# Performance work log

Measured on AMD Instinct MI355X. Metric: run time of the kernel, lower is better.

## Reference

```python
import jax, jax.numpy as jnp
import numpy as np

N = 100000   # num_nodes
E = 1600000  # num_edges
D = 64       # input_dim
H = 64       # hidden_dim
G = 64       # num graphs in batch


def gcn_conv(x, row, col, ew, W, b):
    """PyG GCNConv with edge_weight and self-loops (weight 1.0).
    out = D^{-1/2} (A + I) D^{-1/2} X W + b, aggregating src->dst (row->col)."""
    h = x @ W  # [N, H]
    deg = jax.ops.segment_sum(ew, col, num_segments=N) + 1.0  # self-loop weight 1
    dinv = jnp.where(deg > 0, jax.lax.rsqrt(deg), 0.0)
    norm = dinv[row] * ew * dinv[col]                     # [E]
    agg = jax.ops.segment_sum(h[row] * norm[:, None], col, num_segments=N)
    out = agg + h * (dinv * dinv)[:, None]                # self-loop term
    return out + b


def setup_inputs() -> dict:
    key = jax.random.key(0)
    ks = jax.random.split(key, 20)
    def w(i, shape, fan_in):
        return (jax.random.uniform(ks[i], shape, jnp.float32) * 2.0 - 1.0) / np.sqrt(fan_in)
    inp = {
        "x": jax.random.normal(ks[0], (N, D), jnp.float32),
        "edge_index": jax.random.randint(ks[1], (2, E), 0, N, dtype=jnp.int64),
        "edge_attr": jax.random.uniform(ks[2], (E, 1), jnp.float32),
        "batch": jnp.sort(jax.random.randint(ks[3], (N,), 0, G, dtype=jnp.int64)),
        # GCN layers
        "W0": w(4, (D, H), D), "b0": w(5, (H,), D),
        "W1": w(6, (H, H), H), "b1": w(7, (H,), H),
        "W2": w(8, (H, H), H), "b2": w(9, (H,), H),
        "fc1_w": w(10, (H, H // 2), H), "fc1_b": w(11, (H // 2,), H),
        "fc2_w": w(12, (H // 2, 1), H // 2), "fc2_b": w(13, (1,), H // 2),
        "out_w": w(14, (1, 1), 1), "out_b": w(15, (1,), 1),
    }
    return inp


def reference(x, edge_index, edge_attr, batch, W0, b0, W1, b1, W2, b2,
              fc1_w, fc1_b, fc2_w, fc2_b, out_w, out_b):
    row, col = edge_index[0], edge_index[1]
    ew = edge_attr.reshape(-1)  # edge_attr.view(-1) used as edge_weight
    h = gcn_conv(x, row, col, ew, W0, b0)
    h = jax.nn.relu(h)  # dropout is identity in eval mode
    h = gcn_conv(h, row, col, ew, W1, b1)
    h = jax.nn.relu(h)
    h = gcn_conv(h, row, col, ew, W2, b2)  # no relu after last conv
    # global_mean_pool over batch indices
    sums = jax.ops.segment_sum(h, batch, num_segments=G)            # [G, H]
    cnts = jax.ops.segment_sum(jnp.ones((N,), h.dtype), batch, num_segments=G)
    g = sums / jnp.maximum(cnts, 1.0)[:, None]
    g = jax.nn.relu(g @ fc1_w + fc1_b)
    g = g @ fc2_w + fc2_b                  # [G, 1]
    return g @ out_w + out_b               # [G, 1]
```

## Files before the change

kernel.cpp:

```cpp
#include <hip/hip_runtime.h>
#include <hip/hip_bf16.h>

#define NN 100000
#define NE 1600000
#define DIM 64
#define NG 64

#define NBUK 391
#define EPB 4096
#define NBLK 391

static __device__ __forceinline__ unsigned short bf16bits(float v) {
    __hip_bfloat16 b = __float2bfloat16(v);
    return *reinterpret_cast<unsigned short*>(&b);
}
static __device__ __forceinline__ float bfbits2f(unsigned short u) {
    unsigned int x = ((unsigned int)u) << 16;
    return __uint_as_float(x);
}
static __device__ __forceinline__ void bf2x(unsigned int u, float& lo, float& hi) {
    lo = __uint_as_float(u << 16);
    hi = __uint_as_float(u & 0xFFFF0000u);
}
static __device__ __forceinline__ unsigned csr_pack(int r, float nm) {
    unsigned u = __float_as_uint(nm);
    unsigned nb = ((u + 0x8000u) >> 16) & 0x7FFFu;
    return ((unsigned)r << 15) | nb;
}
static __device__ __forceinline__ float csr_nrm(unsigned u) {
    return __uint_as_float((u & 0x7FFFu) << 16);
}

__global__ __launch_bounds__(1024) void k_ghist2(const int* __restrict__ col,
                                                 int* __restrict__ hist2d,
                                                 int* gcnt, int E) {
    __shared__ int hist[NBUK];
    int t = threadIdx.x;
    for (int i = t; i < NBUK; i += 1024) hist[i] = 0;
    __syncthreads();
    int e0 = blockIdx.x * EPB, e1 = min(e0 + EPB, E);
    for (int e = e0 + t; e < e1; e += 1024) atomicAdd(&hist[col[e] >> 8], 1);
    __syncthreads();
    for (int i = t; i < NBUK; i += 1024) {
        int c = hist[i];
        hist2d[blockIdx.x * NBUK + i] = c;
        if (c) atomicAdd(&gcnt[i], c);
    }
}

__global__ __launch_bounds__(256) void k_gscan(const int* __restrict__ gcnt,
                                               int* __restrict__ boff,
                                               float* __restrict__ sums,
                                               float* __restrict__ cntf) {
    __shared__ int sm[256];
    int t = threadIdx.x;
    for (int i = t; i < NG * DIM; i += 256) sums[i] = 0.f;
    if (t < NG) cntf[t] = 0.f;
    int v0 = (2 * t < NBUK) ? gcnt[2 * t] : 0;
    int v1 = (2 * t + 1 < NBUK) ? gcnt[2 * t + 1] : 0;
    int s = v0 + v1;
    sm[t] = s;
    __syncthreads();
    for (int off = 1; off < 256; off <<= 1) {
        int tmp = (t >= off) ? sm[t - off] : 0;
        __syncthreads();
        sm[t] += tmp;
        __syncthreads();
    }
    int run = sm[t] - s;
    if (2 * t < NBUK) boff[2 * t] = run;
    run += v0;
    if (2 * t + 1 < NBUK) boff[2 * t + 1] = run;
    if (t == 255) boff[NBUK] = run + v1;
}

__global__ __launch_bounds__(256) void k_colscan(const int* __restrict__ hist2d,
                                                 const int* __restrict__ boff,
                                                 int* __restrict__ base2d,
                                                 const float* __restrict__ x,
                                                 unsigned short* __restrict__ xb) {
    __shared__ int sm[256];
    int b = blockIdx.x, t = threadIdx.x;
    int v0 = (2 * t < NBLK) ? hist2d[(size_t)(2 * t) * NBUK + b] : 0;
    int v1 = (2 * t + 1 < NBLK) ? hist2d[(size_t)(2 * t + 1) * NBUK + b] : 0;
    int s = v0 + v1;
    sm[t] = s;
    __syncthreads();
    for (int off = 1; off < 256; off <<= 1) {
        int tmp = (t >= off) ? sm[t - off] : 0;
        __syncthreads();
        sm[t] += tmp;
        __syncthreads();
    }
    int run = boff[b] + sm[t] - s;
    if (2 * t < NBLK) base2d[(size_t)(2 * t) * NBUK + b] = run;
    run += v0;
    if (2 * t + 1 < NBLK) base2d[(size_t)(2 * t + 1) * NBUK + b] = run;
    const int NQ = NN * DIM / 4;
    const int per = (NQ + NBLK - 1) / NBLK;
    int q0 = b * per, q1 = min(q0 + per, NQ);
    for (int i = q0 + t; i < q1; i += 256) {
        float4 v = ((const float4*)x)[i];
        ushort4 o;
        o.x = bf16bits(v.x);
        o.y = bf16bits(v.y);
        o.z = bf16bits(v.z);
        o.w = bf16bits(v.w);
        ((ushort4*)xb)[i] = o;
    }
}

__global__ __launch_bounds__(1024) void k_part1v2(const int* __restrict__ row,
                                                  const int* __restrict__ col,
                                                  const float* __restrict__ ew,
                                                  const int* __restrict__ base2d,
                                                  int2* __restrict__ binned, int E) {
    __shared__ int cur[NBUK];
    int t = threadIdx.x;
    for (int i = t; i < NBUK; i += 1024) cur[i] = base2d[(size_t)blockIdx.x * NBUK + i];
    __syncthreads();
    int e0 = blockIdx.x * EPB, e1 = min(e0 + EPB, E);
    for (int e = e0 + t; e < e1; e += 1024) {
        int c = col[e];
        int b = c >> 8, cl = c & 255;
        int p = atomicAdd(&cur[b], 1);
        binned[p] = make_int2((cl << 17) | row[e], __float_as_int(ew[e]));
    }
}

__global__ __launch_bounds__(256) void k_p2a(const int2* __restrict__ binned,
                                             const int* __restrict__ boff,
                                             float* __restrict__ dinv,
                                             int* __restrict__ rowptr) {
    int b = blockIdx.x, t = threadIdx.x;
    __shared__ unsigned int dsum[256];
    __shared__ int ncnt[256];
    __shared__ int sm[256];
    dsum[t] = 0;
    ncnt[t] = 0;
    __syncthreads();
    int e0 = boff[b], e1 = boff[b + 1];
    for (int e = e0 + t; e < e1; e += 256) {
        int2 v = binned[e];
        int cl = v.x >> 17;
        atomicAdd(&ncnt[cl], 1);
        unsigned int fx = (unsigned int)__float2uint_rn(__int_as_float(v.y) * 16777216.0f);
        atomicAdd(&dsum[cl], fx);
    }
    __syncthreads();
    int c = ncnt[t];
    sm[t] = c;
    __syncthreads();
    for (int off = 1; off < 256; off <<= 1) {
        int tmp = (t >= off) ? sm[t - off] : 0;
        __syncthreads();
        sm[t] += tmp;
        __syncthreads();
    }
    int node = b * 256 + t;
    if (node < NN) {
        rowptr[node] = e0 + sm[t] - c;
        dinv[node] = rsqrtf(1.0f + (float)dsum[t] * (1.0f / 16777216.0f));
    }
    if (b == 0 && t == 0) rowptr[NN] = NE;
}

__global__ __launch_bounds__(256) void k_p2b(const int2* __restrict__ binned,
                                             const int* __restrict__ boff,
                                             const float* __restrict__ dinv,
                                             const int* __restrict__ rowptr,
                                             unsigned* __restrict__ csr) {
    int b = blockIdx.x, t = threadIdx.x;
    __shared__ int ncur[256];
    __shared__ float ldin[256];
    int node = b * 256 + t;
    ncur[t] = (node < NN) ? rowptr[node] : 0;
    ldin[t] = (node < NN) ? dinv[node] : 0.f;
    __syncthreads();
    int e0 = boff[b], e1 = boff[b + 1];
    for (int e = e0 + t; e < e1; e += 256) {
        int2 v = binned[e];
        int cl = v.x >> 17, r = v.x & 0x1FFFF;
        float nm = dinv[r] * __int_as_float(v.y) * ldin[cl];
        int p = atomicAdd(&ncur[cl], 1);
        csr[p] = csr_pack(r, nm);
    }
}

__global__ __launch_bounds__(256, 7) void k_gg(const int* __restrict__ rowptr,
                                               const unsigned* __restrict__ csr,
                                               const uint4* __restrict__ h8,
                                               const float* __restrict__ dinv,
                                               const float* __restrict__ W,
                                               const float* __restrict__ b,
                                               ushort4* __restrict__ out) {
    __shared__ float sW[64][64];
    __shared__ float sX[16][68];
    int tid = threadIdx.x;
#pragma unroll
    for (int i = 0; i < 4; ++i) {
        int q = tid + i * 256;
        ((float4*)&sW[0][0])[q] = ((const float4*)W)[q];
    }
    int node = blockIdx.x * 16 + (tid >> 4);
    int l = tid & 15;
    int g2 = l >> 3, sub = l & 7;
    float acc[8];
#pragma unroll
    for (int i = 0; i < 8; ++i) acc[i] = 0.f;
    if (g2 == 0) {
        float di = dinv[node];
        float s = di * di;
        uint4 v = h8[(size_t)node * 8 + sub];
        float lo, hi;
        bf2x(v.x, lo, hi); acc[0] = lo * s; acc[1] = hi * s;
        bf2x(v.y, lo, hi); acc[2] = lo * s; acc[3] = hi * s;
        bf2x(v.z, lo, hi); acc[4] = lo * s; acc[5] = hi * s;
        bf2x(v.w, lo, hi); acc[6] = lo * s; acc[7] = hi * s;
    }
    int e1 = rowptr[node + 1];
    int e = rowptr[node] + g2;
    unsigned p[4];
#pragma unroll
    for (int i = 0; i < 4; ++i) {
        p[i] = 0u;
        if (e + 2 * i < e1) p[i] = csr[e + 2 * i];
    }
    while (e < e1) {
        uint4 r[4];
#pragma unroll
        for (int i = 0; i < 4; ++i) {
            r[i] = make_uint4(0u, 0u, 0u, 0u);
            if (e + 2 * i < e1) r[i] = h8[(size_t)(p[i] >> 15) * 8 + sub];
        }
        int en = e + 8;
        unsigned q[4];
#pragma unroll
        for (int i = 0; i < 4; ++i) {
            q[i] = 0u;
            if (en + 2 * i < e1) q[i] = csr[en + 2 * i];
        }
#pragma unroll
        for (int i = 0; i < 4; ++i) {
            float nm = csr_nrm(p[i]);
            float lo, hi;
            bf2x(r[i].x, lo, hi); acc[0] = fmaf(lo, nm, acc[0]); acc[1] = fmaf(hi, nm, acc[1]);
            bf2x(r[i].y, lo, hi); acc[2] = fmaf(lo, nm, acc[2]); acc[3] = fmaf(hi, nm, acc[3]);
            bf2x(r[i].z, lo, hi); acc[4] = fmaf(lo, nm, acc[4]); acc[5] = fmaf(hi, nm, acc[5]);
            bf2x(r[i].w, lo, hi); acc[6] = fmaf(lo, nm, acc[6]); acc[7] = fmaf(hi, nm, acc[7]);
        }
#pragma unroll
        for (int i = 0; i < 4; ++i) p[i] = q[i];
        e = en;
    }
#pragma unroll
    for (int i = 0; i < 8; ++i) acc[i] += __shfl_xor(acc[i], 8);
    if (g2 == 0) {
        int c = tid >> 4;
        *(float4*)&sX[c][sub * 8 + 0] = make_float4(acc[0], acc[1], acc[2], acc[3]);
        *(float4*)&sX[c][sub * 8 + 4] = make_float4(acc[4], acc[5], acc[6], acc[7]);
    }
    __syncthreads();
    int nl = tid >> 4, dg = tid & 15;
    float a0 = 0.f, a1 = 0.f, a2 = 0.f, a3 = 0.f;
#pragma unroll 4
    for (int k4 = 0; k4 < 16; ++k4) {
        float4 xr = *(const float4*)&sX[nl][k4 * 4];
        float4 w0 = *(const float4*)&sW[k4 * 4 + 0][dg * 4];
        float4 w1 = *(const float4*)&sW[k4 * 4 + 1][dg * 4];
        float4 w2 = *(const float4*)&sW[k4 * 4 + 2][dg * 4];
        float4 w3 = *(const float4*)&sW[k4 * 4 + 3][dg * 4];
        a0 = fmaf(xr.x, w0.x, a0); a1 = fmaf(xr.x, w0.y, a1);
        a2 = fmaf(xr.x, w0.z, a2); a3 = fmaf(xr.x, w0.w, a3);
        a0 = fmaf(xr.y, w1.x, a0); a1 = fmaf(xr.y, w1.y, a1);
        a2 = fmaf(xr.y, w1.z, a2); a3 = fmaf(xr.y, w1.w, a3);
        a0 = fmaf(xr.z, w2.x, a0); a1 = fmaf(xr.z, w2.y, a1);
        a2 = fmaf(xr.z, w2.z, a2); a3 = fmaf(xr.z, w2.w, a3);
        a0 = fmaf(xr.w, w3.x, a0); a1 = fmaf(xr.w, w3.y, a1);
        a2 = fmaf(xr.w, w3.z, a2); a3 = fmaf(xr.w, w3.w, a3);
    }
    float4 bv = ((const float4*)b)[dg];
    ushort4 o;
    o.x = bf16bits(fmaxf(a0 + bv.x, 0.f));
    o.y = bf16bits(fmaxf(a1 + bv.y, 0.f));
    o.z = bf16bits(fmaxf(a2 + bv.z, 0.f));
    o.w = bf16bits(fmaxf(a3 + bv.w, 0.f));
    out[(size_t)(blockIdx.x * 16 + nl) * 16 + dg] = o;
}

__global__ __launch_bounds__(256) void k_gather5(const int* __restrict__ rowptr,
                                                 const unsigned* __restrict__ csr,
                                                 const uint4* __restrict__ h8,
                                                 const float* __restrict__ dinv,
                                                 uint4* __restrict__ out, int n) {
    int tid = threadIdx.x;
    int node = blockIdx.x * 16 + (tid >> 4);
    if (node >= n) return;
    int l = tid & 15;
    int g2 = l >> 3, sub = l & 7;
    float acc[8];
#pragma unroll
    for (int i = 0; i < 8; ++i) acc[i] = 0.f;
    if (g2 == 0) {
        float di = dinv[node];
        float s = di * di;
        uint4 v = h8[(size_t)node * 8 + sub];
        float lo, hi;
        bf2x(v.x, lo, hi); acc[0] = lo * s; acc[1] = hi * s;
        bf2x(v.y, lo, hi); acc[2] = lo * s; acc[3] = hi * s;
        bf2x(v.z, lo, hi); acc[4] = lo * s; acc[5] = hi * s;
        bf2x(v.w, lo, hi); acc[6] = lo * s; acc[7] = hi * s;
    }
    int e1 = rowptr[node + 1];
    int e = rowptr[node] + g2;
    unsigned p[4];
#pragma unroll
    for (int i = 0; i < 4; ++i) {
        p[i] = 0u;
        if (e + 2 * i < e1) p[i] = csr[e + 2 * i];
    }
    while (e < e1) {
        uint4 r[4];
#pragma unroll
        for (int i = 0; i < 4; ++i) {
            r[i] = make_uint4(0u, 0u, 0u, 0u);
            if (e + 2 * i < e1) r[i] = h8[(size_t)(p[i] >> 15) * 8 + sub];
        }
        int en = e + 8;
        unsigned q[4];
#pragma unroll
        for (int i = 0; i < 4; ++i) {
            q[i] = 0u;
            if (en + 2 * i < e1) q[i] = csr[en + 2 * i];
        }
#pragma unroll
        for (int i = 0; i < 4; ++i) {
            float nm = csr_nrm(p[i]);
            float lo, hi;
            bf2x(r[i].x, lo, hi); acc[0] = fmaf(lo, nm, acc[0]); acc[1] = fmaf(hi, nm, acc[1]);
            bf2x(r[i].y, lo, hi); acc[2] = fmaf(lo, nm, acc[2]); acc[3] = fmaf(hi, nm, acc[3]);
            bf2x(r[i].z, lo, hi); acc[4] = fmaf(lo, nm, acc[4]); acc[5] = fmaf(hi, nm, acc[5]);
            bf2x(r[i].w, lo, hi); acc[6] = fmaf(lo, nm, acc[6]); acc[7] = fmaf(hi, nm, acc[7]);
        }
#pragma unroll
        for (int i = 0; i < 4; ++i) p[i] = q[i];
        e = en;
    }
#pragma unroll
    for (int i = 0; i < 8; ++i) acc[i] += __shfl_xor(acc[i], 8);
    if (g2 == 0) {
        uint4 o;
        o.x = ((unsigned int)bf16bits(acc[1]) << 16) | bf16bits(acc[0]);
        o.y = ((unsigned int)bf16bits(acc[3]) << 16) | bf16bits(acc[2]);
        o.z = ((unsigned int)bf16bits(acc[5]) << 16) | bf16bits(acc[4]);
        o.w = ((unsigned int)bf16bits(acc[7]) << 16) | bf16bits(acc[6]);
        out[(size_t)node * 8 + sub] = o;
    }
}

#define PB3 512
__global__ __launch_bounds__(256) void k_pool3(const int* __restrict__ batch,
                                               const uint4* __restrict__ h8,
                                               float* sums, float* cnt, int n) {
    __shared__ float gsum[64][65];
    __shared__ float gcl[64];
    int t = threadIdx.x;
    for (int i = t; i < 64 * 65; i += 256) (&gsum[0][0])[i] = 0.f;
    if (t < 64) gcl[t] = 0.f;
    __syncthreads();
    int base = blockIdx.x * PB3;
    int end = min(base + PB3, n);
    int g0 = batch[base];
    int cl = t >> 3, sub = t & 7;
    float acc[8];
#pragma unroll
    for (int i = 0; i < 8; ++i) acc[i] = 0.f;
    int gcur = -1, runlen = 0;
    for (int node = base + cl; node < end; node += 32) {
        int g = batch[node];
        if (g != gcur) {
            if (gcur >= 0) {
                int gl = gcur - g0;
#pragma unroll
                for (int i = 0; i < 8; ++i) atomicAdd(&gsum[gl][sub * 8 + i], acc[i]);
                if (sub == 0) atomicAdd(&gcl[gl], (float)runlen);
#pragma unroll
                for (int i = 0; i < 8; ++i) acc[i] = 0.f;
            }
            gcur = g;
            runlen = 0;
        }
        uint4 v = h8[(size_t)node * 8 + sub];
        float lo, hi;
        bf2x(v.x, lo, hi); acc[0] += lo; acc[1] += hi;
        bf2x(v.y, lo, hi); acc[2] += lo; acc[3] += hi;
        bf2x(v.z, lo, hi); acc[4] += lo; acc[5] += hi;
        bf2x(v.w, lo, hi); acc[6] += lo; acc[7] += hi;
        runlen++;
    }
    if (gcur >= 0) {
        int gl = gcur - g0;
#pragma unroll
        for (int i = 0; i < 8; ++i) atomicAdd(&gsum[gl][sub * 8 + i], acc[i]);
        if (sub == 0) atomicAdd(&gcl[gl], (float)runlen);
    }
    __syncthreads();
    int g1 = batch[end - 1];
    int ngr = g1 - g0 + 1;
    for (int idx = t; idx < ngr * 64; idx += 256) {
        int gl = idx >> 6, d = idx & 63;
        float v = gsum[gl][d];
        if (v != 0.f) atomicAdd(&sums[(g0 + gl) * DIM + d], v);
    }
    if (t < ngr) {
        float c = gcl[t];
        if (c != 0.f) atomicAdd(&cnt[g0 + t], c);
    }
}

__global__ __launch_bounds__(64) void k_head(const float* __restrict__ sums,
                                             const float* __restrict__ cnt,
                                             const float* __restrict__ W2,
                                             const float* __restrict__ b2,
                                             const float* __restrict__ fc1w,
                                             const float* __restrict__ fc1b,
                                             const float* __restrict__ fc2w,
                                             const float* __restrict__ fc2b,
                                             const float* __restrict__ ow,
                                             const float* __restrict__ ob,
                                             float* __restrict__ out) {
    int g = blockIdx.x;
    int t = threadIdx.x;
    __shared__ float gv[64];
    __shared__ float tv[64];
    float c = fmaxf(cnt[g], 1.0f);
    gv[t] = sums[g * DIM + t] / c;
    __syncthreads();
    float acc2 = b2[t];
#pragma unroll
    for (int k = 0; k < 64; ++k) acc2 = fmaf(gv[k], W2[k * 64 + t], acc2);
    tv[t] = acc2;
    __syncthreads();
    float r = 0.0f;
    if (t < 32) {
        float acc = fc1b[t];
#pragma unroll
        for (int k = 0; k < 64; ++k) acc = fmaf(tv[k], fc1w[k * 32 + t], acc);
        acc = fmaxf(acc, 0.0f);
        r = acc * fc2w[t];
    }
#pragma unroll
    for (int off = 16; off; off >>= 1) r += __shfl_down(r, off);
    if (t == 0) out[g] = (r + fc2b[0]) * ow[0] + ob[0];
}

extern "C" void kernel_launch(void* const* d_in, const int* in_sizes, int n_in,
                              void* d_out, int out_size, void* d_ws, size_t ws_size,
                              hipStream_t stream) {
    const float* x   = (const float*)d_in[0];
    const int* eidx  = (const int*)d_in[1];
    const float* ew  = (const float*)d_in[2];
    const int* batch = (const int*)d_in[3];
    const float* W0  = (const float*)d_in[4];
    const float* b0  = (const float*)d_in[5];
    const float* W1  = (const float*)d_in[6];
    const float* b1  = (const float*)d_in[7];
    const float* W2  = (const float*)d_in[8];
    const float* b2  = (const float*)d_in[9];
    const float* fc1w = (const float*)d_in[10];
    const float* fc1b = (const float*)d_in[11];
    const float* fc2w = (const float*)d_in[12];
    const float* fc2b = (const float*)d_in[13];
    const float* ow   = (const float*)d_in[14];
    const float* ob   = (const float*)d_in[15];
    float* out = (float*)d_out;

    const int* row = eidx;
    const int* col = eidx + NE;

    char* ws = (char*)d_ws;
    int2* binned           = (int2*)ws;               ws += sizeof(int2) * NE;
    unsigned* csr          = (unsigned*)ws;           ws += sizeof(unsigned) * NE;
    __hip_bfloat16* Xb     = (__hip_bfloat16*)ws;     ws += sizeof(__hip_bfloat16) * (size_t)NN * DIM;
    __hip_bfloat16* Hb     = (__hip_bfloat16*)ws;     ws += sizeof(__hip_bfloat16) * (size_t)NN * DIM;
    int*   hist2d          = (int*)ws;                ws += sizeof(int) * (size_t)NBLK * NBUK;
    int*   base2d          = (int*)ws;                ws += sizeof(int) * (size_t)NBLK * NBUK;
    float* dinv            = (float*)ws;              ws += sizeof(float) * NN;
    int*   rowptr          = (int*)ws;                ws += sizeof(int) * (NN + 1);
    int*   gcnt            = (int*)ws;                ws += sizeof(int) * (NBUK + 1);
    int*   boff            = (int*)ws;                ws += sizeof(int) * (NBUK + 1);
    float* sums            = (float*)ws;              ws += sizeof(float) * NG * DIM;
    float* cntf            = (float*)ws;              ws += sizeof(float) * NG;

    hipMemsetAsync(gcnt, 0, sizeof(int) * NBUK, stream);
    k_ghist2<<<NBLK, 1024, 0, stream>>>(col, hist2d, gcnt, NE);
    k_gscan<<<1, 256, 0, stream>>>(gcnt, boff, sums, cntf);
    k_colscan<<<NBUK, 256, 0, stream>>>(hist2d, boff, base2d, x, (unsigned short*)Xb);
    k_part1v2<<<NBLK, 1024, 0, stream>>>(row, col, ew, base2d, binned, NE);
    k_p2a<<<NBUK, 256, 0, stream>>>(binned, boff, dinv, rowptr);
    k_p2b<<<NBUK, 256, 0, stream>>>(binned, boff, dinv, rowptr, csr);

    int gg_blocks = NN / 16;

    k_gg<<<gg_blocks, 256, 0, stream>>>(rowptr, csr, (const uint4*)Xb, dinv, W0, b0, (ushort4*)Hb);
    k_gg<<<gg_blocks, 256, 0, stream>>>(rowptr, csr, (const uint4*)Hb, dinv, W1, b1, (ushort4*)Xb);

    k_gather5<<<gg_blocks, 256, 0, stream>>>(rowptr, csr, (const uint4*)Xb, dinv, (uint4*)Hb, NN);
    k_pool3<<<(NN + PB3 - 1) / PB3, 256, 0, stream>>>(batch, (const uint4*)Hb, sums, cntf, NN);
    k_head<<<NG, 64, 0, stream>>>(sums, cntf, W2, b2, fc1w, fc1b, fc2w, fc2b, ow, ob, out);
}
```

Baseline: 197.9 us.

## Factor symmetric normalization into node features and merge CSR build kernels

Factors D^{-1/2} A D^{-1/2} into node-side scalings. Features are prescaled by dinv before each gather, the raw edge weight is stored in the CSR, and the sum is rescaled by dinv after aggregation. This removes the random dinv[row] lookup from CSR construction. That lets k_p2a and k_p2b merge into one kernel, which also performs the bf16 conversion of x with dinv applied. The trade-off is extra multiplies per node and a different bf16 rounding point, which could change accuracy slightly.

```diff
diff --git a/kernel.cpp b/kernel.cpp
--- a/kernel.cpp
+++ b/kernel.cpp
@@ -22,12 +22,12 @@
     lo = __uint_as_float(u << 16);
     hi = __uint_as_float(u & 0xFFFF0000u);
 }
-static __device__ __forceinline__ unsigned csr_pack(int r, float nm) {
-    unsigned u = __float_as_uint(nm);
+static __device__ __forceinline__ unsigned csr_pack(int r, float w) {
+    unsigned u = __float_as_uint(w);
     unsigned nb = ((u + 0x8000u) >> 16) & 0x7FFFu;
     return ((unsigned)r << 15) | nb;
 }
-static __device__ __forceinline__ float csr_nrm(unsigned u) {
+static __device__ __forceinline__ float csr_w(unsigned u) {
     return __uint_as_float((u & 0x7FFFu) << 16);
 }
 
@@ -76,9 +76,7 @@
 
 __global__ __launch_bounds__(256) void k_colscan(const int* __restrict__ hist2d,
                                                  const int* __restrict__ boff,
-                                                 int* __restrict__ base2d,
-                                                 const float* __restrict__ x,
-                                                 unsigned short* __restrict__ xb) {
+                                                 int* __restrict__ base2d) {
     __shared__ int sm[256];
     int b = blockIdx.x, t = threadIdx.x;
     int v0 = (2 * t < NBLK) ? hist2d[(size_t)(2 * t) * NBUK + b] : 0;
@@ -96,18 +94,6 @@
     if (2 * t < NBLK) base2d[(size_t)(2 * t) * NBUK + b] = run;
     run += v0;
     if (2 * t + 1 < NBLK) base2d[(size_t)(2 * t + 1) * NBUK + b] = run;
-    const int NQ = NN * DIM / 4;
-    const int per = (NQ + NBLK - 1) / NBLK;
-    int q0 = b * per, q1 = min(q0 + per, NQ);
-    for (int i = q0 + t; i < q1; i += 256) {
-        float4 v = ((const float4*)x)[i];
-        ushort4 o;
-        o.x = bf16bits(v.x);
-        o.y = bf16bits(v.y);
-        o.z = bf16bits(v.z);
-        o.w = bf16bits(v.w);
-        ((ushort4*)xb)[i] = o;
-    }
 }
 
 __global__ __launch_bounds__(1024) void k_part1v2(const int* __restrict__ row,
@@ -128,14 +114,19 @@
     }
 }
 
-__global__ __launch_bounds__(256) void k_p2a(const int2* __restrict__ binned,
-                                             const int* __restrict__ boff,
-                                             float* __restrict__ dinv,
-                                             int* __restrict__ rowptr) {
+__global__ __launch_bounds__(256) void k_p2(const int2* __restrict__ binned,
+                                            const int* __restrict__ boff,
+                                            float* __restrict__ dinv,
+                                            int* __restrict__ rowptr,
+                                            unsigned* __restrict__ csr,
+                                            const float* __restrict__ x,
+                                            unsigned short* __restrict__ xb) {
     int b = blockIdx.x, t = threadIdx.x;
     __shared__ unsigned int dsum[256];
     __shared__ int ncnt[256];
     __shared__ int sm[256];
+    __shared__ float ldin[256];
+    __shared__ int ncur[256];
     dsum[t] = 0;
     ncnt[t] = 0;
     __syncthreads();
@@ -158,32 +149,34 @@
         __syncthreads();
     }
     int node = b * 256 + t;
+    float dv = rsqrtf(1.0f + (float)dsum[t] * (1.0f / 16777216.0f));
+    int rp = e0 + sm[t] - c;
+    ldin[t] = dv;
+    ncur[t] = rp;
     if (node < NN) {
-        rowptr[node] = e0 + sm[t] - c;
-        dinv[node] = rsqrtf(1.0f + (float)dsum[t] * (1.0f / 16777216.0f));
+        rowptr[node] = rp;
+        dinv[node] = dv;
     }
     if (b == 0 && t == 0) rowptr[NN] = NE;
-}
-
-__global__ __launch_bounds__(256) void k_p2b(const int2* __restrict__ binned,
-                                             const int* __restrict__ boff,
-                                             const float* __restrict__ dinv,
-                                             const int* __restrict__ rowptr,
-                                             unsigned* __restrict__ csr) {
-    int b = blockIdx.x, t = threadIdx.x;
-    __shared__ int ncur[256];
-    __shared__ float ldin[256];
-    int node = b * 256 + t;
-    ncur[t] = (node < NN) ? rowptr[node] : 0;
-    ldin[t] = (node < NN) ? dinv[node] : 0.f;
-    __syncthreads();
-    int e0 = boff[b], e1 = boff[b + 1];
+    __syncthreads();
     for (int e = e0 + t; e < e1; e += 256) {
         int2 v = binned[e];
         int cl = v.x >> 17, r = v.x & 0x1FFFF;
-        float nm = dinv[r] * __int_as_float(v.y) * ldin[cl];
         int p = atomicAdd(&ncur[cl], 1);
-        csr[p] = csr_pack(r, nm);
+        csr[p] = csr_pack(r, __int_as_float(v.y));
+    }
+    int nfirst = b * 256;
+    int nlast = min(nfirst + 256, NN);
+    for (int idx = t; idx < (nlast - nfirst) * 16; idx += 256) {
+        int nl = idx >> 4, q = idx & 15;
+        float dvn = ldin[nl];
+        float4 v = ((const float4*)x)[(size_t)(nfirst + nl) * 16 + q];
+        ushort4 o;
+        o.x = bf16bits(v.x * dvn);
+        o.y = bf16bits(v.y * dvn);
+        o.z = bf16bits(v.z * dvn);
+        o.w = bf16bits(v.w * dvn);
+        ((ushort4*)xb)[(size_t)(nfirst + nl) * 16 + q] = o;
     }
 }
 
@@ -205,18 +198,17 @@
     int node = blockIdx.x * 16 + (tid >> 4);
     int l = tid & 15;
     int g2 = l >> 3, sub = l & 7;
+    float dv = dinv[node];
     float acc[8];
 #pragma unroll
     for (int i = 0; i < 8; ++i) acc[i] = 0.f;
     if (g2 == 0) {
-        float di = dinv[node];
-        float s = di * di;
         uint4 v = h8[(size_t)node * 8 + sub];
         float lo, hi;
-        bf2x(v.x, lo, hi); acc[0] = lo * s; acc[1] = hi * s;
-        bf2x(v.y, lo, hi); acc[2] = lo * s; acc[3] = hi * s;
-        bf2x(v.z, lo, hi); acc[4] = lo * s; acc[5] = hi * s;
-        bf2x(v.w, lo, hi); acc[6] = lo * s; acc[7] = hi * s;
+        bf2x(v.x, lo, hi); acc[0] = lo; acc[1] = hi;
+        bf2x(v.y, lo, hi); acc[2] = lo; acc[3] = hi;
+        bf2x(v.z, lo, hi); acc[4] = lo; acc[5] = hi;
+        bf2x(v.w, lo, hi); acc[6] = lo; acc[7] = hi;
     }
     int e1 = rowptr[node + 1];
     int e = rowptr[node] + g2;
@@ -242,7 +234,7 @@
         }
 #pragma unroll
         for (int i = 0; i < 4; ++i) {
-            float nm = csr_nrm(p[i]);
+            float nm = csr_w(p[i]);
             float lo, hi;
             bf2x(r[i].x, lo, hi); acc[0] = fmaf(lo, nm, acc[0]); acc[1] = fmaf(hi, nm, acc[1]);
             bf2x(r[i].y, lo, hi); acc[2] = fmaf(lo, nm, acc[2]); acc[3] = fmaf(hi, nm, acc[3]);
@@ -257,8 +249,8 @@
     for (int i = 0; i < 8; ++i) acc[i] += __shfl_xor(acc[i], 8);
     if (g2 == 0) {
         int c = tid >> 4;
-        *(float4*)&sX[c][sub * 8 + 0] = make_float4(acc[0], acc[1], acc[2], acc[3]);
-        *(float4*)&sX[c][sub * 8 + 4] = make_float4(acc[4], acc[5], acc[6], acc[7]);
+        *(float4*)&sX[c][sub * 8 + 0] = make_float4(acc[0] * dv, acc[1] * dv, acc[2] * dv, acc[3] * dv);
+        *(float4*)&sX[c][sub * 8 + 4] = make_float4(acc[4] * dv, acc[5] * dv, acc[6] * dv, acc[7] * dv);
     }
     __syncthreads();
     int nl = tid >> 4, dg = tid & 15;
@@ -281,14 +273,14 @@
     }
     float4 bv = ((const float4*)b)[dg];
     ushort4 o;
-    o.x = bf16bits(fmaxf(a0 + bv.x, 0.f));
-    o.y = bf16bits(fmaxf(a1 + bv.y, 0.f));
-    o.z = bf16bits(fmaxf(a2 + bv.z, 0.f));
-    o.w = bf16bits(fmaxf(a3 + bv.w, 0.f));
+    o.x = bf16bits(fmaxf(a0 + bv.x, 0.f) * dv);
+    o.y = bf16bits(fmaxf(a1 + bv.y, 0.f) * dv);
+    o.z = bf16bits(fmaxf(a2 + bv.z, 0.f) * dv);
+    o.w = bf16bits(fmaxf(a3 + bv.w, 0.f) * dv);
     out[(size_t)(blockIdx.x * 16 + nl) * 16 + dg] = o;
 }
 
-__global__ __launch_bounds__(256) void k_gather5(const int* __restrict__ rowptr,
+__global__ __launch_bounds__(256) void k_gather6(const int* __restrict__ rowptr,
                                                  const unsigned* __restrict__ csr,
                                                  const uint4* __restrict__ h8,
                                                  const float* __restrict__ dinv,
@@ -298,18 +290,17 @@
     if (node >= n) return;
     int l = tid & 15;
     int g2 = l >> 3, sub = l & 7;
+    float dv = dinv[node];
     float acc[8];
 #pragma unroll
     for (int i = 0; i < 8; ++i) acc[i] = 0.f;
     if (g2 == 0) {
-        float di = dinv[node];
-        float s = di * di;
         uint4 v = h8[(size_t)node * 8 + sub];
         float lo, hi;
-        bf2x(v.x, lo, hi); acc[0] = lo * s; acc[1] = hi * s;
-        bf2x(v.y, lo, hi); acc[2] = lo * s; acc[3] = hi * s;
-        bf2x(v.z, lo, hi); acc[4] = lo * s; acc[5] = hi * s;
-        bf2x(v.w, lo, hi); acc[6] = lo * s; acc[7] = hi * s;
+        bf2x(v.x, lo, hi); acc[0] = lo; acc[1] = hi;
+        bf2x(v.y, lo, hi); acc[2] = lo; acc[3] = hi;
+        bf2x(v.z, lo, hi); acc[4] = lo; acc[5] = hi;
+        bf2x(v.w, lo, hi); acc[6] = lo; acc[7] = hi;
     }
     int e1 = rowptr[node + 1];
     int e = rowptr[node] + g2;
@@ -335,7 +326,7 @@
         }
 #pragma unroll
         for (int i = 0; i < 4; ++i) {
-            float nm = csr_nrm(p[i]);
+            float nm = csr_w(p[i]);
             float lo, hi;
             bf2x(r[i].x, lo, hi); acc[0] = fmaf(lo, nm, acc[0]); acc[1] = fmaf(hi, nm, acc[1]);
             bf2x(r[i].y, lo, hi); acc[2] = fmaf(lo, nm, acc[2]); acc[3] = fmaf(hi, nm, acc[3]);
@@ -350,10 +341,10 @@
     for (int i = 0; i < 8; ++i) acc[i] += __shfl_xor(acc[i], 8);
     if (g2 == 0) {
         uint4 o;
-        o.x = ((unsigned int)bf16bits(acc[1]) << 16) | bf16bits(acc[0]);
-        o.y = ((unsigned int)bf16bits(acc[3]) << 16) | bf16bits(acc[2]);
-        o.z = ((unsigned int)bf16bits(acc[5]) << 16) | bf16bits(acc[4]);
-        o.w = ((unsigned int)bf16bits(acc[7]) << 16) | bf16bits(acc[6]);
+        o.x = ((unsigned int)bf16bits(acc[1] * dv) << 16) | bf16bits(acc[0] * dv);
+        o.y = ((unsigned int)bf16bits(acc[3] * dv) << 16) | bf16bits(acc[2] * dv);
+        o.z = ((unsigned int)bf16bits(acc[5] * dv) << 16) | bf16bits(acc[4] * dv);
+        o.w = ((unsigned int)bf16bits(acc[7] * dv) << 16) | bf16bits(acc[6] * dv);
         out[(size_t)node * 8 + sub] = o;
     }
 }
@@ -495,17 +486,16 @@
     hipMemsetAsync(gcnt, 0, sizeof(int) * NBUK, stream);
     k_ghist2<<<NBLK, 1024, 0, stream>>>(col, hist2d, gcnt, NE);
     k_gscan<<<1, 256, 0, stream>>>(gcnt, boff, sums, cntf);
-    k_colscan<<<NBUK, 256, 0, stream>>>(hist2d, boff, base2d, x, (unsigned short*)Xb);
+    k_colscan<<<NBUK, 256, 0, stream>>>(hist2d, boff, base2d);
     k_part1v2<<<NBLK, 1024, 0, stream>>>(row, col, ew, base2d, binned, NE);
-    k_p2a<<<NBUK, 256, 0, stream>>>(binned, boff, dinv, rowptr);
-    k_p2b<<<NBUK, 256, 0, stream>>>(binned, boff, dinv, rowptr, csr);
+    k_p2<<<NBUK, 256, 0, stream>>>(binned, boff, dinv, rowptr, csr, x, (unsigned short*)Xb);
 
     int gg_blocks = NN / 16;
 
     k_gg<<<gg_blocks, 256, 0, stream>>>(rowptr, csr, (const uint4*)Xb, dinv, W0, b0, (ushort4*)Hb);
     k_gg<<<gg_blocks, 256, 0, stream>>>(rowptr, csr, (const uint4*)Hb, dinv, W1, b1, (ushort4*)Xb);
 
-    k_gather5<<<gg_blocks, 256, 0, stream>>>(rowptr, csr, (const uint4*)Xb, dinv, (uint4*)Hb, NN);
+    k_gather6<<<gg_blocks, 256, 0, stream>>>(rowptr, csr, (const uint4*)Xb, dinv, (uint4*)Hb, NN);
     k_pool3<<<(NN + PB3 - 1) / PB3, 256, 0, stream>>>(batch, (const uint4*)Hb, sums, cntf, NN);
     k_head<<<NG, 64, 0, stream>>>(sums, cntf, W2, b2, fc1w, fc1b, fc2w, fc2b, ow, ob, out);
 }
```

New measurement: 187.4 us. -5.3%, faster.
